# Optimization experiments

Hardware: AMD Instinct MI355X
Metric: run time of the kernel (lower is better)

Reference implementation:

```python
import jax, jax.numpy as jnp
import numpy as np

CHANNELS = 512
GROUPS = 32
EPS = 1e-6


def setup_inputs() -> dict:
    key = jax.random.key(0)
    ks = jax.random.split(key, 10)
    C = CHANNELS
    s = 1.0 / np.sqrt(C)
    return {
        "hidden_states": jax.random.normal(ks[0], (4, 64, 64, C), dtype=jnp.float32),
        "gn_scale": jnp.ones((C,), dtype=jnp.float32),
        "gn_bias": jnp.zeros((C,), dtype=jnp.float32),
        "wq": jax.random.normal(ks[1], (C, C), dtype=jnp.float32) * s,
        "bq": jnp.zeros((C,), dtype=jnp.float32),
        "wk": jax.random.normal(ks[2], (C, C), dtype=jnp.float32) * s,
        "bk": jnp.zeros((C,), dtype=jnp.float32),
        "wv": jax.random.normal(ks[3], (C, C), dtype=jnp.float32) * s,
        "bv": jnp.zeros((C,), dtype=jnp.float32),
        "wo": jax.random.normal(ks[4], (C, C), dtype=jnp.float32) * s,
        "bo": jnp.zeros((C,), dtype=jnp.float32),
    }


def reference(hidden_states, gn_scale, gn_bias, wq, bq, wk, bk, wv, bv, wo, bo):
    B, H, W, C = hidden_states.shape
    residual = hidden_states
    L = H * W
    x = hidden_states.reshape(B, L, C)

    # GroupNorm: stats over (spatial, channels-within-group), per batch per group
    xg = x.reshape(B, L, GROUPS, C // GROUPS)
    mean = jnp.mean(xg, axis=(1, 3), keepdims=True)
    var = jnp.var(xg, axis=(1, 3), keepdims=True)
    xn = ((xg - mean) * jax.lax.rsqrt(var + EPS)).reshape(B, L, C)
    xn = xn * gn_scale + gn_bias

    # QKV projections (heads=1, head_dim=C)
    q = xn @ wq + bq
    k = xn @ wk + bk
    v = xn @ wv + bv

    scale = 1.0 / jnp.sqrt(jnp.asarray(C, dtype=q.dtype))
    scores = jnp.einsum('bld,bsd->bls', q, k) * scale  # [B, L, L]
    attn = jax.nn.softmax(scores, axis=-1)
    out = jnp.einsum('bls,bsd->bld', attn, v)

    out = out @ wo + bo
    return out.reshape(B, H, W, C) + residual
```

## Files before the change

### kernel.cpp

```cpp
#include <hip/hip_runtime.h>
#include <hip/hip_bf16.h>
#include <stdint.h>

#define BATCH 4
#define SEQ   4096
#define CH    512
#define NGRP  32
#define GEPS  1e-6f

typedef short  short8  __attribute__((ext_vector_type(8)));
typedef float  floatx4 __attribute__((ext_vector_type(4)));
typedef long   longx2  __attribute__((ext_vector_type(2)));

static __device__ __forceinline__ short bf16b(float f) {
    __hip_bfloat16 h = __float2bfloat16(f);
    return __builtin_bit_cast(short, h);
}
static __device__ __forceinline__ float bf2f(short s) {
    unsigned u = ((unsigned)(unsigned short)s) << 16;
    return __builtin_bit_cast(float, u);
}
static __device__ __forceinline__ char fp8b(float f) {
    int pk = __builtin_amdgcn_cvt_pk_fp8_f32(f, f, 0, false);
    return (char)(pk & 0xff);
}

static __device__ __forceinline__ void dma16(const void* g, void* l) {
    __builtin_amdgcn_global_load_lds(
        (const __attribute__((address_space(1))) unsigned int*)g,
        (__attribute__((address_space(3))) unsigned int*)l, 16, 0, 0);
}

static __device__ __forceinline__ float rowmax16(float x) {
    int xi = __builtin_bit_cast(int, x);
    x = fmaxf(x, __builtin_bit_cast(float, __builtin_amdgcn_update_dpp(xi, xi, 0x128, 0xf, 0xf, true)));
    xi = __builtin_bit_cast(int, x);
    x = fmaxf(x, __builtin_bit_cast(float, __builtin_amdgcn_update_dpp(xi, xi, 0x124, 0xf, 0xf, true)));
    xi = __builtin_bit_cast(int, x);
    x = fmaxf(x, __builtin_bit_cast(float, __builtin_amdgcn_update_dpp(xi, xi, 0x122, 0xf, 0xf, true)));
    xi = __builtin_bit_cast(int, x);
    x = fmaxf(x, __builtin_bit_cast(float, __builtin_amdgcn_update_dpp(xi, xi, 0x121, 0xf, 0xf, true)));
    return x;
}

__global__ __launch_bounds__(256) void gn_wt_kernel(const float* __restrict__ x,
                                                    float* __restrict__ statsraw,
                                                    const float* __restrict__ w0,
                                                    const float* __restrict__ w1,
                                                    const float* __restrict__ w2,
                                                    const float* __restrict__ w3,
                                                    short* __restrict__ wT) {
    __shared__ float a1[256], a2[256];
    __shared__ float trs[32][33];
    int blk = blockIdx.x;
    int t = threadIdx.x;
    if (blk < 256) {
        size_t row0 = (size_t)blk * 64;
        int qd = t & 127;
        int rh = t >> 7;
        const float* base = x + row0 * 512 + qd * 4;
        float s1 = 0.f, s2 = 0.f;
        #pragma unroll 4
        for (int i = 0; i < 32; ++i) {
            int r = rh + i * 2;
            float4 v = *reinterpret_cast<const float4*>(base + (size_t)r * 512);
            s1 += v.x + v.y + v.z + v.w;
            s2 += v.x * v.x + v.y * v.y + v.z * v.z + v.w * v.w;
        }
        a1[t] = s1; a2[t] = s2;
        __syncthreads();
        if (t < 32) {
            float u1 = 0.f, u2 = 0.f;
            #pragma unroll
            for (int e = 0; e < 4; ++e) {
                u1 += a1[t * 4 + e] + a1[128 + t * 4 + e];
                u2 += a2[t * 4 + e] + a2[128 + t * 4 + e];
            }
            int b = (int)(row0 >> 12);
            atomicAdd(&statsraw[(b * 32 + t) * 2],     u1);
            atomicAdd(&statsraw[(b * 32 + t) * 2 + 1], u2);
        }
    } else {
        int bz = (blk - 256) >> 8;
        int rem = (blk - 256) & 255;
        int n0 = (rem & 15) * 32, k0 = (rem >> 4) * 32;
        const float* w = (bz == 0) ? w0 : (bz == 1) ? w1 : (bz == 2) ? w2 : w3;
        short* out = wT + (size_t)bz * CH * CH;
        int tx = t & 31, ty = t >> 5;
        #pragma unroll
        for (int i = 0; i < 4; ++i) {
            int kk = ty + i * 8;
            trs[kk][tx] = w[(size_t)(k0 + kk) * CH + n0 + tx];
        }
        __syncthreads();
        #pragma unroll
        for (int i = 0; i < 4; ++i) {
            int nn = ty + i * 8;
            out[(size_t)(n0 + nn) * CH + k0 + tx] = bf16b(trs[tx][nn]);
        }
    }
}

__global__ __launch_bounds__(256) void gn_apply_kernel(const float* __restrict__ x,
                                                       const float* __restrict__ statsraw,
                                                       const float* __restrict__ gsc,
                                                       const float* __restrict__ gbs,
                                                       short* __restrict__ xn) {
    int i4 = blockIdx.x * 256 + threadIdx.x;
    int base = i4 * 4;
    int b = base >> 21;
    int c = base & 511;
    int sidx = (b * 32 + (c >> 4)) * 2;
    float s1 = statsraw[sidx], s2 = statsraw[sidx + 1];
    float mean = s1 * (1.f / 65536.f);
    float var  = s2 * (1.f / 65536.f) - mean * mean;
    float rstd = rsqrtf(var + GEPS);
    float4 xv = reinterpret_cast<const float4*>(x)[i4];
    float4 sv = *reinterpret_cast<const float4*>(gsc + c);
    float4 bv = *reinterpret_cast<const float4*>(gbs + c);
    union { short s[4]; uint2 u; } p;
    p.s[0] = bf16b((xv.x - mean) * rstd * sv.x + bv.x);
    p.s[1] = bf16b((xv.y - mean) * rstd * sv.y + bv.y);
    p.s[2] = bf16b((xv.z - mean) * rstd * sv.z + bv.z);
    p.s[3] = bf16b((xv.w - mean) * rstd * sv.w + bv.w);
    reinterpret_cast<uint2*>(xn)[i4] = p.u;
}

__global__ __launch_bounds__(256) void gemm_qkv_kernel(const short* __restrict__ A,
                                                       const short* __restrict__ wT,
                                                       const float* __restrict__ bq,
                                                       const float* __restrict__ bk,
                                                       const float* __restrict__ bv,
                                                       char* __restrict__ q8,
                                                       char* __restrict__ k8,
                                                       char* __restrict__ vT8) {
    __shared__ short As[128 * 64];
    __shared__ short Bs[128 * 64];
    __shared__ char  vls[128 * 144];
    int m0 = blockIdx.x * 128;
    int nblk = blockIdx.y;
    int which = nblk >> 2;
    int n0 = (nblk & 3) * 128;
    const short* BT = wT + (size_t)which * 512 * 512;
    const float* bias = (which == 0) ? bq : (which == 1) ? bk : bv;
    int t = threadIdx.x;
    int w = t >> 6, lane = t & 63;
    int wr = w >> 1, wc = w & 1;
    int l15 = lane & 15, l4 = lane >> 4;
    floatx4 acc[4][4];
    #pragma unroll
    for (int i = 0; i < 4; ++i)
        #pragma unroll
        for (int j = 0; j < 4; ++j) acc[i][j] = (floatx4){0.f, 0.f, 0.f, 0.f};

    for (int k0 = 0; k0 < 512; k0 += 64) {
        __syncthreads();
        #pragma unroll
        for (int i = 0; i < 4; ++i) {
            int c = i * 256 + t;
            int row = c >> 3, j = (c & 7) ^ (row & 7);
            dma16(&A[(size_t)(m0 + row) * 512 + k0 + j * 8], &As[(c & ~63) * 8]);
            dma16(&BT[(size_t)(n0 + row) * 512 + k0 + j * 8], &Bs[(c & ~63) * 8]);
        }
        __syncthreads();
        #pragma unroll
        for (int kk = 0; kk < 64; kk += 32) {
            short8 af[4], bf[4];
            #pragma unroll
            for (int i = 0; i < 4; ++i) {
                int row = wr * 64 + i * 16 + l15;
                int j = (kk >> 3) + l4;
                af[i] = *reinterpret_cast<const short8*>(&As[(row * 8 + (j ^ (l15 & 7))) * 8]);
            }
            #pragma unroll
            for (int j2 = 0; j2 < 4; ++j2) {
                int row = wc * 64 + j2 * 16 + l15;
                int j = (kk >> 3) + l4;
                bf[j2] = *reinterpret_cast<const short8*>(&Bs[(row * 8 + (j ^ (l15 & 7))) * 8]);
            }
            #pragma unroll
            for (int i = 0; i < 4; ++i)
                #pragma unroll
                for (int j2 = 0; j2 < 4; ++j2)
                    acc[i][j2] = __builtin_amdgcn_mfma_f32_16x16x32_bf16(af[i], bf[j2], acc[i][j2], 0, 0, 0);
        }
    }
    if (which == 0) {
        #pragma unroll
        for (int i = 0; i < 4; ++i)
            #pragma unroll
            for (int j = 0; j < 4; ++j)
                #pragma unroll
                for (int r = 0; r < 4; ++r) {
                    int rl = wr * 64 + i * 16 + l4 * 4 + r;
                    int cl = wc * 64 + j * 16 + l15;
                    vls[rl * 144 + cl] = fp8b(acc[i][j][r] + bias[n0 + cl]);
                }
        __syncthreads();
        #pragma unroll
        for (int p = 0; p < 4; ++p) {
            int slot = p * 256 + t;
            int c = slot >> 3, off = (slot & 7) * 16;
            uint4 v;
            __builtin_memcpy(&v, &vls[c * 144 + off], 16);
            *reinterpret_cast<uint4*>(&q8[(size_t)(m0 + c) * 512 + n0 + off]) = v;
        }
    } else if (which == 1) {
        #pragma unroll
        for (int i = 0; i < 4; ++i)
            #pragma unroll
            for (int j = 0; j < 4; ++j)
                #pragma unroll
                for (int r = 0; r < 4; ++r) {
                    int rl = wr * 64 + i * 16 + l4 * 4 + r;
                    int cl = wc * 64 + j * 16 + l15;
                    int sblk = rl >> 5, srow = rl & 15, hp = (rl >> 4) & 1;
                    int ch = (cl >> 3) ^ (srow & 7);
                    vls[sblk * 4096 + srow * 256 + ch * 16 + hp * 8 + (cl & 7)]
                        = fp8b(acc[i][j][r] + bias[n0 + cl]);
                }
        __syncthreads();
        int bb = m0 >> 12, sb0 = (m0 & 4095) >> 5;
        #pragma unroll
        for (int p = 0; p < 4; ++p) {
            int u = p * 256 + t;
            int sblk = u >> 8, srow = (u >> 4) & 15, ch = u & 15;
            uint4 v;
            __builtin_memcpy(&v, &vls[sblk * 4096 + srow * 256 + ((ch ^ (srow & 7)) * 16)], 16);
            char* dst = k8 + (size_t)bb * 2097152 + (size_t)(sb0 + sblk) * 16384
                      + srow * 1024 + n0 * 2 + ch * 16;
            *reinterpret_cast<uint4*>(dst) = v;
        }
    } else {
        __syncthreads();
        #pragma unroll
        for (int i = 0; i < 4; ++i)
            #pragma unroll
            for (int j = 0; j < 4; ++j)
                #pragma unroll
                for (int r = 0; r < 4; ++r) {
                    int rl = wr * 64 + i * 16 + l4 * 4 + r;
                    int rp = (rl & ~31) | (((rl & 15) << 1) | ((rl >> 4) & 1));
                    int cl = wc * 64 + j * 16 + l15;
                    vls[cl * 144 + rp] = fp8b(acc[i][j][r] + bias[n0 + cl]);
                }
        __syncthreads();
        int b = m0 >> 12, l0 = m0 & 4095;
        #pragma unroll
        for (int p = 0; p < 4; ++p) {
            int slot = p * 256 + t;
            int c = slot >> 3, off = (slot & 7) * 16;
            uint4 v;
            __builtin_memcpy(&v, &vls[c * 144 + off], 16);
            int dcol = n0 + c;
            int g = dcol >> 5, rr = dcol & 15, h = (dcol >> 4) & 1;
            int s = l0 + off;
            int sb = s >> 5, mb = (s & 31) >> 3;
            char* dst = vT8 + (size_t)b * 2097152 + (size_t)sb * 16384
                      + (size_t)((((g * 16 + rr) * 4 + mb) * 16) + h * 8);
            unsigned long long lo = ((unsigned long long)v.y << 32) | v.x;
            unsigned long long hi = ((unsigned long long)v.w << 32) | v.z;
            *reinterpret_cast<unsigned long long*>(dst)      = lo;
            *reinterpret_cast<unsigned long long*>(dst + 16) = hi;
        }
    }
}

__global__ __launch_bounds__(256) void gemm_bt_kernel(const short* __restrict__ Opart,
                                                      const float* __restrict__ ml,
                                                      const short* __restrict__ BT,
                                                      const float* __restrict__ bias,
                                                      float* __restrict__ outf,
                                                      const float* __restrict__ resid) {
    __shared__ short As[128 * 64];
    __shared__ short Bs[128 * 64];
    int m0 = blockIdx.x * 128, n0 = blockIdx.y * 128;
    int t = threadIdx.x;
    int w = t >> 6, lane = t & 63;
    int wr = w >> 1, wc = w & 1;
    int l15 = lane & 15, l4 = lane >> 4;
    const size_t PART = (size_t)BATCH * SEQ;
    floatx4 acc[4][4];
    #pragma unroll
    for (int i = 0; i < 4; ++i)
        #pragma unroll
        for (int j = 0; j < 4; ++j) acc[i][j] = (floatx4){0.f, 0.f, 0.f, 0.f};

    for (int k0 = 0; k0 < 512; k0 += 64) {
        __syncthreads();
        #pragma unroll
        for (int i = 0; i < 4; ++i) {
            int c = i * 256 + t;
            int rl = c >> 3, j = (c & 7) ^ (rl & 7);
            size_t rowg = (size_t)(m0 + rl);
            const short* s0 = Opart + rowg * 512 + k0 + j * 8;
            const short* s1 = s0 + PART * 512;
            uint4 a0 = *reinterpret_cast<const uint4*>(s0);
            uint4 a1 = *reinterpret_cast<const uint4*>(s1);
            float mA = ml[rowg * 2],          lA = ml[rowg * 2 + 1];
            float mB = ml[(PART + rowg) * 2], lB = ml[(PART + rowg) * 2 + 1];
            float mm = fmaxf(mA, mB);
            float e0 = exp2f(mA - mm), e1 = exp2f(mB - mm);
            float inv = 1.f / (e0 * lA + e1 * lB);
            e0 *= inv; e1 *= inv;
            union { uint4 u; short s[8]; } ua, ub, uo;
            ua.u = a0; ub.u = a1;
            #pragma unroll
            for (int e = 0; e < 8; ++e)
                uo.s[e] = bf16b(bf2f(ua.s[e]) * e0 + bf2f(ub.s[e]) * e1);
            *reinterpret_cast<uint4*>(&As[c * 8]) = uo.u;
            dma16(&BT[(size_t)(n0 + rl) * 512 + k0 + j * 8], &Bs[(c & ~63) * 8]);
        }
        __syncthreads();
        #pragma unroll
        for (int kk = 0; kk < 64; kk += 32) {
            short8 af[4], bf[4];
            #pragma unroll
            for (int i = 0; i < 4; ++i) {
                int row = wr * 64 + i * 16 + l15;
                int j = (kk >> 3) + l4;
                af[i] = *reinterpret_cast<const short8*>(&As[(row * 8 + (j ^ (l15 & 7))) * 8]);
            }
            #pragma unroll
            for (int j2 = 0; j2 < 4; ++j2) {
                int row = wc * 64 + j2 * 16 + l15;
                int j = (kk >> 3) + l4;
                bf[j2] = *reinterpret_cast<const short8*>(&Bs[(row * 8 + (j ^ (l15 & 7))) * 8]);
            }
            #pragma unroll
            for (int i = 0; i < 4; ++i)
                #pragma unroll
                for (int j2 = 0; j2 < 4; ++j2)
                    acc[i][j2] = __builtin_amdgcn_mfma_f32_16x16x32_bf16(af[i], bf[j2], acc[i][j2], 0, 0, 0);
        }
    }
    #pragma unroll
    for (int i = 0; i < 4; ++i)
        #pragma unroll
        for (int j = 0; j < 4; ++j)
            #pragma unroll
            for (int r = 0; r < 4; ++r) {
                int row = m0 + wr * 64 + i * 16 + l4 * 4 + r;
                int col = n0 + wc * 64 + j * 16 + l15;
                float vv = acc[i][j][r] + bias[col];
                outf[(size_t)row * 512 + col] = vv + resid[(size_t)row * 512 + col];
            }
}

__global__ __launch_bounds__(512, 1) void flash_kernel(const char* __restrict__ q8,
                                                       const char* __restrict__ k8,
                                                       const char* __restrict__ v8,
                                                       short* __restrict__ Opart,
                                                       float* __restrict__ ml) {
    __shared__ __align__(16) char smem[70656];
    int bx = blockIdx.x;
    int pb = bx & 7;
    int part = pb >> 2, b = pb & 3;
    int q0 = (bx >> 3) * 128;
    int t = threadIdx.x, w = t >> 6, lane = t & 63;
    int l15 = lane & 15, l4 = lane >> 4;
    const float c2 = 0.06375873735f;
    const float MARGIN = 7.2134752f;

    long qf[16];
    {
        const char* qrow = q8 + ((size_t)b * SEQ + q0 + w * 16 + l15) * 512;
        #pragma unroll
        for (int ks = 0; ks < 16; ++ks)
            qf[ks] = *reinterpret_cast<const long*>(qrow + ks * 32 + l4 * 8);
    }

    floatx4 acc[32];
    #pragma unroll
    for (int i = 0; i < 32; ++i) acc[i] = (floatx4){0.f, 0.f, 0.f, 0.f};
    floatx4 lacc = (floatx4){0.f, 0.f, 0.f, 0.f};
    float mused[4] = {-1e30f, -1e30f, -1e30f, -1e30f};

    const long ones = 0x3838383838383838L;

    const char* kbase = k8 + (size_t)b * SEQ * 512;
    const char* vbase = v8 + (size_t)b * 512 * SEQ;
    const int sb0 = part * 64;

    const int ksw = l15 & 7;
    const int vsw = (l15 >> 1) & 3;
    const char* kA_E = smem + ((l15 * 64 + (l4 ^ ksw)) << 4);
    const char* kA_O = smem + ((l15 * 64 + ((4 + l4) ^ ksw)) << 4);
    const char* vA   = smem + 32768 + ((l15 * 4 + (l4 ^ vsw)) << 4);
    char* Ps = smem + 65536 + w * 640;

    int kSrc[2], vSrc[2];
    #pragma unroll
    for (int i = 0; i < 2; ++i) {
        int c = i * 512 + t;
        kSrc[i] = (((c & ~63) | ((c & 63) ^ ((c >> 6) & 7))) << 4);
        vSrc[i] = (((c & ~3)  | ((c & 3)  ^ ((c >> 3) & 3))) << 4);
    }
    const int ldsD = (t & ~63) << 4;

    auto stage = [&](int sb, int buf) {
        const char* kt = kbase + (size_t)sb * 16384;
        const char* vt = vbase + (size_t)sb * 16384;
        char* Kd = smem + buf * 16384 + ldsD;
        char* Vd = smem + 32768 + buf * 16384 + ldsD;
        #pragma unroll
        for (int i = 0; i < 2; ++i) dma16(kt + kSrc[i], Kd + i * 8192);
        #pragma unroll
        for (int i = 0; i < 2; ++i) dma16(vt + vSrc[i], Vd + i * 8192);
    };

    stage(sb0, 0);
    __syncthreads();

    for (int it = 0; it < 64; ++it) {
        int cur = it & 1;
        int coff = cur << 14;
        if (it + 1 < 64) stage(sb0 + it + 1, 1 - cur);

        floatx4 sa0 = (floatx4){0.f, 0.f, 0.f, 0.f};
        floatx4 sa1 = (floatx4){0.f, 0.f, 0.f, 0.f};
        #pragma unroll
        for (int j = 0; j < 8; ++j) {
            longx2 kE = *reinterpret_cast<const longx2*>(kA_E + coff + j * 128);
            longx2 kO = *reinterpret_cast<const longx2*>(kA_O + coff + j * 128);
            sa0 = __builtin_amdgcn_mfma_f32_16x16x32_fp8_fp8(qf[2 * j],     kE[0], sa0, 0, 0, 0);
            sa1 = __builtin_amdgcn_mfma_f32_16x16x32_fp8_fp8(qf[2 * j],     kE[1], sa1, 0, 0, 0);
            sa0 = __builtin_amdgcn_mfma_f32_16x16x32_fp8_fp8(qf[2 * j + 1], kO[0], sa0, 0, 0, 0);
            sa1 = __builtin_amdgcn_mfma_f32_16x16x32_fp8_fp8(qf[2 * j + 1], kO[1], sa1, 0, 0, 0);
        }

        float v0[4], v1[4], nm4[4];
        bool need = false;
        #pragma unroll
        for (int r = 0; r < 4; ++r) {
            v0[r] = sa0[r] * c2; v1[r] = sa1[r] * c2;
            nm4[r] = rowmax16(fmaxf(v0[r], v1[r]));
            need |= (nm4[r] > mused[r] + MARGIN);
        }
        if (__ballot(need)) {
            #pragma unroll
            for (int r = 0; r < 4; ++r) {
                float nm = fmaxf(mused[r], nm4[r]);
                float al = exp2f(mused[r] - nm);
                lacc[r] *= al;
                #pragma unroll
                for (int i = 0; i < 32; ++i) acc[i][r] *= al;
                mused[r] = nm;
            }
        }
        #pragma unroll
        for (int r = 0; r < 4; ++r) {
            int pk = __builtin_amdgcn_cvt_pk_fp8_f32(exp2f(v0[r] - mused[r]),
                                                     exp2f(v1[r] - mused[r]), 0, false);
            *reinterpret_cast<short*>(Ps + (l4 * 4 + r) * 40 + l15 * 2) = (short)pk;
        }

        long pf;
        __builtin_memcpy(&pf, (const char*)__builtin_assume_aligned(Ps + l15 * 40 + l4 * 8, 8), 8);
        lacc = __builtin_amdgcn_mfma_f32_16x16x32_fp8_fp8(pf, ones, lacc, 0, 0, 0);
        #pragma unroll
        for (int g = 0; g < 16; ++g) {
            longx2 vv = *reinterpret_cast<const longx2*>(vA + coff + g * 1024);
            acc[2 * g]     = __builtin_amdgcn_mfma_f32_16x16x32_fp8_fp8(pf, vv[0], acc[2 * g],     0, 0, 0);
            acc[2 * g + 1] = __builtin_amdgcn_mfma_f32_16x16x32_fp8_fp8(pf, vv[1], acc[2 * g + 1], 0, 0, 0);
        }

        __syncthreads();
    }

    short* obase = Opart + (((size_t)part * BATCH + b) * SEQ + q0 + w * 16) * 512;
    #pragma unroll
    for (int r = 0; r < 4; ++r) {
        #pragma unroll
        for (int tt = 0; tt < 32; ++tt)
            obase[(size_t)(l4 * 4 + r) * 512 + tt * 16 + l15] = bf16b(acc[tt][r]);
    }
    if (l15 == 0) {
        #pragma unroll
        for (int r = 0; r < 4; ++r) {
            size_t rowg = ((size_t)part * BATCH + b) * SEQ + q0 + w * 16 + l4 * 4 + r;
            ml[rowg * 2]     = mused[r];
            ml[rowg * 2 + 1] = lacc[r];
        }
    }
}

extern "C" void kernel_launch(void* const* d_in, const int* in_sizes, int n_in,
                              void* d_out, int out_size, void* d_ws, size_t ws_size,
                              hipStream_t stream) {
    const float* x   = (const float*)d_in[0];
    const float* gsc = (const float*)d_in[1];
    const float* gbs = (const float*)d_in[2];
    const float* wq  = (const float*)d_in[3];
    const float* bq  = (const float*)d_in[4];
    const float* wk  = (const float*)d_in[5];
    const float* bk  = (const float*)d_in[6];
    const float* wv  = (const float*)d_in[7];
    const float* bv  = (const float*)d_in[8];
    const float* wo  = (const float*)d_in[9];
    const float* bo  = (const float*)d_in[10];
    float* out = (float*)d_out;

    char* ws = (char*)d_ws;
    const size_t MB = 1ull << 20;
    short* xn    = (short*)ws;
    char*  q8    = (char*)(ws + 16 * MB);
    char*  k8    = (char*)(ws + 24 * MB);
    char*  vT8   = (char*)(ws + 32 * MB);
    short* Opart = (short*)(ws + 40 * MB);
    short* wT    = (short*)(ws + 72 * MB);
    float* stats = (float*)(ws + 74 * MB);
    float* ml    = (float*)(ws + 74 * MB + 65536);

    hipMemsetAsync(stats, 0, 256 * sizeof(float), stream);
    gn_wt_kernel<<<1280, 256, 0, stream>>>(x, stats, wq, wk, wv, wo, wT);
    gn_apply_kernel<<<8192, 256, 0, stream>>>(x, stats, gsc, gbs, xn);

    short* woT = wT + 786432;

    gemm_qkv_kernel<<<dim3(128, 12), 256, 0, stream>>>(xn, wT, bq, bk, bv, q8, k8, vT8);
    flash_kernel<<<256, 512, 0, stream>>>(q8, k8, vT8, Opart, ml);
    gemm_bt_kernel<<<dim3(128, 4), 256, 0, stream>>>(Opart, ml, woT, bo, out, x);
}
```

Baseline: 288.8 us.

## Process two KV tiles per flash iteration and hoist merge weights in output GEMM

The flash attention loop now stages and consumes two 32-key K/V tiles per iteration, doubling shared memory buffers and halving the number of iterations and block-wide barriers. Softmax max/rescale checks are amortized over 64 keys instead of 32. Separately, the output-projection kernel hoists the per-row partial-merge weights (exp/reciprocal from ml) out of the k-loop so they are computed once. The larger LDS footprint (~138KB) limits occupancy to one block per CU and increases register pressure.

```diff
diff --git a/kernel.cpp b/kernel.cpp
--- a/kernel.cpp
+++ b/kernel.cpp
@@ -286,6 +286,19 @@
         #pragma unroll
         for (int j = 0; j < 4; ++j) acc[i][j] = (floatx4){0.f, 0.f, 0.f, 0.f};
 
+    float e0h[4], e1h[4];
+    #pragma unroll
+    for (int i = 0; i < 4; ++i) {
+        int rl = (i * 256 + t) >> 3;
+        size_t rowg = (size_t)(m0 + rl);
+        float mA = ml[rowg * 2],          lA = ml[rowg * 2 + 1];
+        float mB = ml[(PART + rowg) * 2], lB = ml[(PART + rowg) * 2 + 1];
+        float mm = fmaxf(mA, mB);
+        float e0 = exp2f(mA - mm), e1 = exp2f(mB - mm);
+        float inv = 1.f / (e0 * lA + e1 * lB);
+        e0h[i] = e0 * inv; e1h[i] = e1 * inv;
+    }
+
     for (int k0 = 0; k0 < 512; k0 += 64) {
         __syncthreads();
         #pragma unroll
@@ -297,17 +310,11 @@
             const short* s1 = s0 + PART * 512;
             uint4 a0 = *reinterpret_cast<const uint4*>(s0);
             uint4 a1 = *reinterpret_cast<const uint4*>(s1);
-            float mA = ml[rowg * 2],          lA = ml[rowg * 2 + 1];
-            float mB = ml[(PART + rowg) * 2], lB = ml[(PART + rowg) * 2 + 1];
-            float mm = fmaxf(mA, mB);
-            float e0 = exp2f(mA - mm), e1 = exp2f(mB - mm);
-            float inv = 1.f / (e0 * lA + e1 * lB);
-            e0 *= inv; e1 *= inv;
             union { uint4 u; short s[8]; } ua, ub, uo;
             ua.u = a0; ub.u = a1;
             #pragma unroll
             for (int e = 0; e < 8; ++e)
-                uo.s[e] = bf16b(bf2f(ua.s[e]) * e0 + bf2f(ub.s[e]) * e1);
+                uo.s[e] = bf16b(bf2f(ua.s[e]) * e0h[i] + bf2f(ub.s[e]) * e1h[i]);
             *reinterpret_cast<uint4*>(&As[c * 8]) = uo.u;
             dma16(&BT[(size_t)(n0 + rl) * 512 + k0 + j * 8], &Bs[(c & ~63) * 8]);
         }
@@ -352,7 +359,7 @@
                                                        const char* __restrict__ v8,
                                                        short* __restrict__ Opart,
                                                        float* __restrict__ ml) {
-    __shared__ __align__(16) char smem[70656];
+    __shared__ __align__(16) char smem[141312];
     int bx = blockIdx.x;
     int pb = bx & 7;
     int part = pb >> 2, b = pb & 3;
@@ -386,55 +393,65 @@
     const int vsw = (l15 >> 1) & 3;
     const char* kA_E = smem + ((l15 * 64 + (l4 ^ ksw)) << 4);
     const char* kA_O = smem + ((l15 * 64 + ((4 + l4) ^ ksw)) << 4);
-    const char* vA   = smem + 32768 + ((l15 * 4 + (l4 ^ vsw)) << 4);
-    char* Ps = smem + 65536 + w * 640;
-
-    int kSrc[2], vSrc[2];
-    #pragma unroll
-    for (int i = 0; i < 2; ++i) {
+    const char* vA   = smem + 65536 + ((l15 * 4 + (l4 ^ vsw)) << 4);
+    char* Ps = smem + 131072 + w * 1280;
+
+    int kSrc[4], vSrc[4];
+    #pragma unroll
+    for (int i = 0; i < 4; ++i) {
         int c = i * 512 + t;
-        kSrc[i] = (((c & ~63) | ((c & 63) ^ ((c >> 6) & 7))) << 4);
-        vSrc[i] = (((c & ~3)  | ((c & 3)  ^ ((c >> 3) & 3))) << 4);
+        int tile = c >> 10, cw = c & 1023;
+        kSrc[i] = tile * 16384 + (((cw & ~63) | ((cw & 63) ^ ((cw >> 6) & 7))) << 4);
+        vSrc[i] = tile * 16384 + (((cw & ~3)  | ((cw & 3)  ^ ((cw >> 3) & 3))) << 4);
     }
     const int ldsD = (t & ~63) << 4;
 
     auto stage = [&](int sb, int buf) {
         const char* kt = kbase + (size_t)sb * 16384;
         const char* vt = vbase + (size_t)sb * 16384;
-        char* Kd = smem + buf * 16384 + ldsD;
-        char* Vd = smem + 32768 + buf * 16384 + ldsD;
-        #pragma unroll
-        for (int i = 0; i < 2; ++i) dma16(kt + kSrc[i], Kd + i * 8192);
-        #pragma unroll
-        for (int i = 0; i < 2; ++i) dma16(vt + vSrc[i], Vd + i * 8192);
+        char* Kd = smem + buf * 32768 + ldsD;
+        char* Vd = smem + 65536 + buf * 32768 + ldsD;
+        #pragma unroll
+        for (int i = 0; i < 4; ++i) dma16(kt + kSrc[i], Kd + i * 8192);
+        #pragma unroll
+        for (int i = 0; i < 4; ++i) dma16(vt + vSrc[i], Vd + i * 8192);
     };
 
     stage(sb0, 0);
     __syncthreads();
 
-    for (int it = 0; it < 64; ++it) {
+    for (int it = 0; it < 32; ++it) {
         int cur = it & 1;
-        int coff = cur << 14;
-        if (it + 1 < 64) stage(sb0 + it + 1, 1 - cur);
-
-        floatx4 sa0 = (floatx4){0.f, 0.f, 0.f, 0.f};
-        floatx4 sa1 = (floatx4){0.f, 0.f, 0.f, 0.f};
+        int coff = cur << 15;
+        if (it + 1 < 32) stage(sb0 + 2 * (it + 1), 1 - cur);
+
+        floatx4 s00 = (floatx4){0.f, 0.f, 0.f, 0.f};
+        floatx4 s01 = (floatx4){0.f, 0.f, 0.f, 0.f};
+        floatx4 s10 = (floatx4){0.f, 0.f, 0.f, 0.f};
+        floatx4 s11 = (floatx4){0.f, 0.f, 0.f, 0.f};
         #pragma unroll
         for (int j = 0; j < 8; ++j) {
-            longx2 kE = *reinterpret_cast<const longx2*>(kA_E + coff + j * 128);
-            longx2 kO = *reinterpret_cast<const longx2*>(kA_O + coff + j * 128);
-            sa0 = __builtin_amdgcn_mfma_f32_16x16x32_fp8_fp8(qf[2 * j],     kE[0], sa0, 0, 0, 0);
-            sa1 = __builtin_amdgcn_mfma_f32_16x16x32_fp8_fp8(qf[2 * j],     kE[1], sa1, 0, 0, 0);
-            sa0 = __builtin_amdgcn_mfma_f32_16x16x32_fp8_fp8(qf[2 * j + 1], kO[0], sa0, 0, 0, 0);
-            sa1 = __builtin_amdgcn_mfma_f32_16x16x32_fp8_fp8(qf[2 * j + 1], kO[1], sa1, 0, 0, 0);
-        }
-
-        float v0[4], v1[4], nm4[4];
+            longx2 kE0 = *reinterpret_cast<const longx2*>(kA_E + coff + j * 128);
+            longx2 kO0 = *reinterpret_cast<const longx2*>(kA_O + coff + j * 128);
+            longx2 kE1 = *reinterpret_cast<const longx2*>(kA_E + coff + 16384 + j * 128);
+            longx2 kO1 = *reinterpret_cast<const longx2*>(kA_O + coff + 16384 + j * 128);
+            s00 = __builtin_amdgcn_mfma_f32_16x16x32_fp8_fp8(qf[2 * j],     kE0[0], s00, 0, 0, 0);
+            s01 = __builtin_amdgcn_mfma_f32_16x16x32_fp8_fp8(qf[2 * j],     kE0[1], s01, 0, 0, 0);
+            s10 = __builtin_amdgcn_mfma_f32_16x16x32_fp8_fp8(qf[2 * j],     kE1[0], s10, 0, 0, 0);
+            s11 = __builtin_amdgcn_mfma_f32_16x16x32_fp8_fp8(qf[2 * j],     kE1[1], s11, 0, 0, 0);
+            s00 = __builtin_amdgcn_mfma_f32_16x16x32_fp8_fp8(qf[2 * j + 1], kO0[0], s00, 0, 0, 0);
+            s01 = __builtin_amdgcn_mfma_f32_16x16x32_fp8_fp8(qf[2 * j + 1], kO0[1], s01, 0, 0, 0);
+            s10 = __builtin_amdgcn_mfma_f32_16x16x32_fp8_fp8(qf[2 * j + 1], kO1[0], s10, 0, 0, 0);
+            s11 = __builtin_amdgcn_mfma_f32_16x16x32_fp8_fp8(qf[2 * j + 1], kO1[1], s11, 0, 0, 0);
+        }
+
+        float v00[4], v01[4], v10[4], v11[4], nm4[4];
         bool need = false;
         #pragma unroll
         for (int r = 0; r < 4; ++r) {
-            v0[r] = sa0[r] * c2; v1[r] = sa1[r] * c2;
-            nm4[r] = rowmax16(fmaxf(v0[r], v1[r]));
+            v00[r] = s00[r] * c2; v01[r] = s01[r] * c2;
+            v10[r] = s10[r] * c2; v11[r] = s11[r] * c2;
+            nm4[r] = rowmax16(fmaxf(fmaxf(v00[r], v01[r]), fmaxf(v10[r], v11[r])));
             need |= (nm4[r] > mused[r] + MARGIN);
         }
         if (__ballot(need)) {
@@ -450,19 +467,30 @@
         }
         #pragma unroll
         for (int r = 0; r < 4; ++r) {
-            int pk = __builtin_amdgcn_cvt_pk_fp8_f32(exp2f(v0[r] - mused[r]),
-                                                     exp2f(v1[r] - mused[r]), 0, false);
-            *reinterpret_cast<short*>(Ps + (l4 * 4 + r) * 40 + l15 * 2) = (short)pk;
-        }
-
-        long pf;
-        __builtin_memcpy(&pf, (const char*)__builtin_assume_aligned(Ps + l15 * 40 + l4 * 8, 8), 8);
-        lacc = __builtin_amdgcn_mfma_f32_16x16x32_fp8_fp8(pf, ones, lacc, 0, 0, 0);
+            int pk0 = __builtin_amdgcn_cvt_pk_fp8_f32(exp2f(v00[r] - mused[r]),
+                                                      exp2f(v01[r] - mused[r]), 0, false);
+            int pk1 = __builtin_amdgcn_cvt_pk_fp8_f32(exp2f(v10[r] - mused[r]),
+                                                      exp2f(v11[r] - mused[r]), 0, false);
+            *reinterpret_cast<short*>(Ps + (l4 * 4 + r) * 40 + l15 * 2)       = (short)pk0;
+            *reinterpret_cast<short*>(Ps + 640 + (l4 * 4 + r) * 40 + l15 * 2) = (short)pk1;
+        }
+
+        long pf0, pf1;
+        __builtin_memcpy(&pf0, (const char*)__builtin_assume_aligned(Ps + l15 * 40 + l4 * 8, 8), 8);
+        __builtin_memcpy(&pf1, (const char*)__builtin_assume_aligned(Ps + 640 + l15 * 40 + l4 * 8, 8), 8);
+        lacc = __builtin_amdgcn_mfma_f32_16x16x32_fp8_fp8(pf0, ones, lacc, 0, 0, 0);
+        lacc = __builtin_amdgcn_mfma_f32_16x16x32_fp8_fp8(pf1, ones, lacc, 0, 0, 0);
         #pragma unroll
         for (int g = 0; g < 16; ++g) {
-            longx2 vv = *reinterpret_cast<const longx2*>(vA + coff + g * 1024);
-            acc[2 * g]     = __builtin_amdgcn_mfma_f32_16x16x32_fp8_fp8(pf, vv[0], acc[2 * g],     0, 0, 0);
-            acc[2 * g + 1] = __builtin_amdgcn_mfma_f32_16x16x32_fp8_fp8(pf, vv[1], acc[2 * g + 1], 0, 0, 0);
+            longx2 va = *reinterpret_cast<const longx2*>(vA + coff + g * 1024);
+            acc[2 * g]     = __builtin_amdgcn_mfma_f32_16x16x32_fp8_fp8(pf0, va[0], acc[2 * g],     0, 0, 0);
+            acc[2 * g + 1] = __builtin_amdgcn_mfma_f32_16x16x32_fp8_fp8(pf0, va[1], acc[2 * g + 1], 0, 0, 0);
+        }
+        #pragma unroll
+        for (int g = 0; g < 16; ++g) {
+            longx2 vb = *reinterpret_cast<const longx2*>(vA + coff + 16384 + g * 1024);
+            acc[2 * g]     = __builtin_amdgcn_mfma_f32_16x16x32_fp8_fp8(pf1, vb[0], acc[2 * g],     0, 0, 0);
+            acc[2 * g + 1] = __builtin_amdgcn_mfma_f32_16x16x32_fp8_fp8(pf1, vb[1], acc[2 * g + 1], 0, 0, 0);
         }
 
         __syncthreads();
```

Measured after the change: 277.6 us. -3.9%, faster.
